# Kernel optimization log

Hardware: AMD Instinct MI355X
Metric: run time of the kernel (lower is better)

The kernel has to match this reference:

```python
import jax, jax.numpy as jnp
import numpy as np
import math

RCR = 5.2
RCA = 3.5
NUM_SPECIES = 4


def _triu_index(num_species):
    s1, s2 = np.triu_indices(num_species)
    ret = np.zeros((num_species, num_species), dtype=np.int32)
    ret[s1, s2] = np.arange(len(s1))
    ret[s2, s1] = np.arange(len(s1))
    return ret


def _cutoff_cosine(d, rc):
    return 0.5 * jnp.cos(d * (math.pi / rc)) + 0.5


def setup_inputs():
    key = jax.random.key(0)
    k1, k2 = jax.random.split(key)
    M, A = 32, 48
    BOX = 8.0  # ~0.43 atoms/A^3, realistic organic density
    coordinates = jax.random.uniform(k1, (M, A, 3), dtype=jnp.float32) * BOX
    species = jax.random.randint(k2, (M, A), 0, NUM_SPECIES)
    EtaR = jnp.array([16.0], dtype=jnp.float32)
    ShfR = jnp.asarray(0.9 + (RCR - 0.9) / 16.0 * np.arange(16), dtype=jnp.float32)
    EtaA = jnp.array([8.0], dtype=jnp.float32)
    Zeta = jnp.array([32.0], dtype=jnp.float32)
    ShfA = jnp.asarray(0.9 + (RCA - 0.9) / 4.0 * np.arange(4), dtype=jnp.float32)
    ShfZ = jnp.asarray((np.arange(8) + 0.5) * np.pi / 8.0, dtype=jnp.float32)
    return {"coordinates": coordinates, "EtaR": EtaR, "ShfR": ShfR,
            "EtaA": EtaA, "Zeta": Zeta, "ShfA": ShfA, "ShfZ": ShfZ,
            "species": species}


def _compute_aev(coordinates, EtaR, ShfR, EtaA, Zeta, ShfA, ShfZ, species):
    M, A, _ = coordinates.shape
    S = NUM_SPECIES
    npairs_sp = S * (S + 1) // 2  # 10 unordered species pairs
    rad_sub = EtaR.shape[0] * ShfR.shape[0]   # 16
    ang_sub = EtaA.shape[0] * Zeta.shape[0] * ShfA.shape[0] * ShfZ.shape[0]  # 32

    diff = coordinates[:, :, None, :] - coordinates[:, None, :, :]  # (M,A,A,3)
    D = jnp.linalg.norm(diff, axis=-1)                              # (M,A,A)
    mrow = jnp.arange(M)[:, None]

    # ---------- radial AEV (eq. 3) ----------
    p1, p2 = np.triu_indices(A, 1)                                  # static (P,)
    d = D[:, p1, p2]                                                # (M,P)
    mask_r = (d <= RCR).astype(d.dtype)
    du = d[:, :, None, None]                                        # (M,P,1,1)
    fc = _cutoff_cosine(du, RCR)
    rt = 0.25 * jnp.exp(-EtaR[:, None] * (du - ShfR[None, :]) ** 2) * fc
    rt = (rt * mask_r[:, :, None, None]).reshape(M, len(p1), rad_sub)
    sp = species
    idx1 = p1[None, :] * S + sp[:, p2]                              # (M,P)
    idx2 = p2[None, :] * S + sp[:, p1]
    radial = jnp.zeros((M, A * S, rad_sub), dtype=rt.dtype)
    radial = radial.at[mrow, idx1].add(rt).at[mrow, idx2].add(rt)
    radial = radial.reshape(M, A, S * rad_sub)

    # ---------- angular AEV (eq. 4) ----------
    # static triple list: central atom i with unordered neighbor pair (j,k), j,k != i
    jj, kk = np.triu_indices(A - 1, 1)
    tri = []
    for i in range(A):
        others = np.concatenate([np.arange(i), np.arange(i + 1, A)])
        tri.append(np.stack([np.full(jj.shape, i), others[jj], others[kk]], 1))
    tri = np.concatenate(tri)                                       # (T,3)
    ci, n1, n2 = tri[:, 0], tri[:, 1], tri[:, 2]

    v1 = coordinates[:, n1] - coordinates[:, ci]                    # (M,T,3)
    v2 = coordinates[:, n2] - coordinates[:, ci]
    d1 = D[:, ci, n1]
    d2 = D[:, ci, n2]
    mask_a = ((d1 <= RCA) & (d2 <= RCA)).astype(d1.dtype)           # (M,T)
    eps = 1e-8  # torch cosine_similarity eps
    cos = 0.95 * jnp.sum(v1 * v2, -1) / (jnp.maximum(d1, eps) * jnp.maximum(d2, eps))
    ang = jnp.arccos(cos)                                           # (M,T)

    # broadcast axes: (M, T, EtaA, Zeta, ShfA, ShfZ) as in torchani constants
    EtaA_b = EtaA.reshape(1, 1, -1, 1, 1, 1)
    Zeta_b = Zeta.reshape(1, 1, 1, -1, 1, 1)
    ShfA_b = ShfA.reshape(1, 1, 1, 1, -1, 1)
    ShfZ_b = ShfZ.reshape(1, 1, 1, 1, 1, -1)
    a6 = ang[:, :, None, None, None, None]
    dm = ((d1 + d2) / 2)[:, :, None, None, None, None]
    fcj = (_cutoff_cosine(d1, RCA) * _cutoff_cosine(d2, RCA))[:, :, None, None, None, None]
    f1 = ((1 + jnp.cos(a6 - ShfZ_b)) / 2) ** Zeta_b
    f2 = jnp.exp(-EtaA_b * (dm - ShfA_b) ** 2)
    at = (2 * f1 * f2 * fcj).reshape(M, tri.shape[0], ang_sub)
    at = at * mask_a[:, :, None]

    triu = jnp.asarray(_triu_index(S))
    pidx = triu[sp[:, n1], sp[:, n2]]                               # (M,T)
    flat = ci[None, :] * npairs_sp + pidx
    angular = jnp.zeros((M, A * npairs_sp, ang_sub), dtype=at.dtype)
    angular = angular.at[mrow, flat].add(at).reshape(M, A, npairs_sp * ang_sub)

    return jnp.concatenate([radial, angular], axis=-1)              # (M,A,384)


def reference(coordinates, EtaR, ShfR, EtaA, Zeta, ShfA, ShfZ, species):
    return _compute_aev(coordinates, EtaR, ShfR, EtaA, Zeta, ShfA, ShfZ, species)
```

## Files before the change

### kernel.cpp

```cpp
#include <hip/hip_runtime.h>
#include <hip/hip_bf16.h>


#define NA 48
#define RCR_F 5.2f
#define RCA_F 3.5f
#define PI_F 3.14159265358979f
#define LOG2E_F 1.44269504088896f
#define RADLEN 64
#define AEVLEN 384

struct Smem {
    float sx[NA], sy[NA], sz[NA];
    int   ssp[NA];
    float2 rab[NA];
    float ad[NA], avx[NA], avy[NA], avz[NA], afc[NA]; int asp[NA];
    int   nR, nAn;
    float4 pstage[256];
    int    bins[10], start[10];
    float rpart[4][64];
    float apart[4][320];
};

template <typename T> __device__ __forceinline__ float toF(const T* p, int i);
template <> __device__ __forceinline__ float toF<float>(const float* p, int i) { return p[i]; }
template <> __device__ __forceinline__ float toF<__hip_bfloat16>(const __hip_bfloat16* p, int i) { return __bfloat162float(p[i]); }

template <typename T> __device__ __forceinline__ void stF(T* p, size_t i, float v);
template <> __device__ __forceinline__ void stF<float>(float* p, size_t i, float v) { p[i] = v; }
template <> __device__ __forceinline__ void stF<__hip_bfloat16>(__hip_bfloat16* p, size_t i, float v) { p[i] = __float2bfloat16(v); }

__device__ __forceinline__ int triu_idx(int a, int b) {
    int lo = a < b ? a : b;
    int hi = a < b ? b : a;
    return lo * 4 - (lo * (lo - 1)) / 2 + (hi - lo);
}

template <typename T>
__device__ void aev_body(Smem& sm,
    const T* __restrict__ coords, const T* __restrict__ etaR_p,
    const T* __restrict__ shfR_p, const T* __restrict__ etaA_p,
    const T* __restrict__ zeta_p, const T* __restrict__ shfA_p,
    const T* __restrict__ shfZ_p, const int* __restrict__ species,
    T* __restrict__ out)
{
    const int tid  = threadIdx.x;
    const int lane = tid & 63;
    const int w    = tid >> 6;
    const int bid  = blockIdx.x;
    const int m  = bid / NA;
    const int ci = bid % NA;

    const float etaR = toF(etaR_p, 0);
    const float etaA = toF(etaA_p, 0);
    const float zeta = toF(zeta_p, 0);
    const float kR   = etaR * LOG2E_F;
    const float k2   = etaA * LOG2E_F;

    if (tid < NA) {
        int g = m * NA + tid;
        sm.sx[tid]  = toF(coords, 3 * g + 0);
        sm.sy[tid]  = toF(coords, 3 * g + 1);
        sm.sz[tid]  = toF(coords, 3 * g + 2);
        sm.ssp[tid] = species[g];
    }
    __syncthreads();

    if (w == 0) {
        const float cx = sm.sx[ci], cy = sm.sy[ci], cz = sm.sz[ci];
        float dx = 0.f, dy = 0.f, dz = 0.f, d = 1e30f;
        if (lane < NA && lane != ci) {
            dx = sm.sx[lane] - cx; dy = sm.sy[lane] - cy; dz = sm.sz[lane] - cz;
            d = sqrtf(dx * dx + dy * dy + dz * dz);
        }
        unsigned long long mR = __ballot(d <= RCR_F);
        unsigned long long mA = __ballot(d <= RCA_F);
        unsigned long long lanebit = 1ull << lane;
        unsigned long long below = lanebit - 1ull;
        if (mR & lanebit) {
            int s = __popcll(mR & below);
            float fcR = 0.5f * __cosf(d * (PI_F / RCR_F)) + 0.5f;
            float rb = fmaxf(__log2f(0.25f * fcR) - kR * d * d, -8.0e4f);
            unsigned rbu = (__float_as_uint(rb) & ~3u) | (unsigned)sm.ssp[lane];
            sm.rab[s] = make_float2(2.f * kR * d, __uint_as_float(rbu));
        }
        if (mA & lanebit) {
            int s = __popcll(mA & below);
            sm.ad[s]  = d;
            sm.avx[s] = dx; sm.avy[s] = dy; sm.avz[s] = dz;
            sm.afc[s] = 0.5f * __cosf(d * (PI_F / RCA_F)) + 0.5f;
            sm.asp[s] = sm.ssp[lane];
        }
        if (lane == 0) { sm.nR = (int)__popcll(mR); sm.nAn = (int)__popcll(mA); }
    }
    __syncthreads();

    const int nR  = sm.nR;
    const int nAn = sm.nAn;

    const float myShfR = toF(shfR_p, lane & 15);
    const int   mySp   = lane >> 4;
    const float myRc   = kR * myShfR * myShfR;
    const bool  z32    = (zeta == 32.f);

    float racc = 0.f;
    for (int i = w; i < nR; i += 4) {
        float2 rv = sm.rab[i];
        unsigned ru = __float_as_uint(rv.y);
        float arg = __builtin_fmaf(rv.x, myShfR, rv.y) - myRc;
        float t = __builtin_amdgcn_exp2f(arg);
        racc += ((int)(ru & 3u) == mySp) ? t : 0.f;
    }
    sm.rpart[w][lane] = racc;

    const int myA  = (lane >> 3) & 3;
    const int myZ  = lane & 7;
    const int p0   = lane >> 5;
    const float myShfA = toF(shfA_p, myA);
    const float myShfZ = toF(shfZ_p, myZ);
    const float myCz = __cosf(myShfZ);
    const float mySz = __sinf(myShfZ);
    const float myLc = k2 * myShfA * myShfA;

    float accs[5] = {0.f, 0.f, 0.f, 0.f, 0.f};
    const int np = nAn * (nAn - 1) / 2;

    for (int c0 = 0; c0 < np; c0 += 256) {
        const int nc = (np - c0 < 256) ? (np - c0) : 256;
        if (tid < 10) sm.bins[tid] = 0;
        __syncthreads();

        int myrow = -1, myrank = 0;
        float4 P4;
        if (tid < nc) {
            int p = c0 + tid;
            const int b = 2 * nAn - 1;
            float s = sqrtf((float)(b * b - 8 * p));
            int j = (int)(((float)b - s) * 0.5f);
            if ((j + 1) * (b - 1 - j) <= 2 * p) j++;
            if (j * (b - j) > 2 * p) j--;
            int k = p - ((j * (b - j)) >> 1) + j + 1;

            float d1 = sm.ad[j], d2 = sm.ad[k];
            float dot = sm.avx[j] * sm.avx[k] + sm.avy[j] * sm.avy[k] + sm.avz[j] * sm.avz[k];
            float cv = 0.95f * dot / (fmaxf(d1, 1e-8f) * fmaxf(d2, 1e-8f));
            float sv = sqrtf(fmaxf(1.f - cv * cv, 0.f));
            float dm = 0.5f * (d1 + d2);
            float fc2 = 2.f * sm.afc[j] * sm.afc[k];
            float pe = fmaxf(-k2 * dm * dm + __log2f(fc2), -8.0e4f);
            float pd = 2.f * k2 * dm;
            P4 = make_float4(cv, sv, pd, pe);
            myrow = triu_idx(sm.asp[j], sm.asp[k]);
            myrank = atomicAdd(&sm.bins[myrow], 1);
        }
        __syncthreads();
        if (tid == 0) {
            int s = 0;
            #pragma unroll
            for (int r = 0; r < 10; r++) { sm.start[r] = s; s += sm.bins[r]; }
        }
        __syncthreads();
        if (myrow >= 0) sm.pstage[sm.start[myrow] + myrank] = P4;
        __syncthreads();

        #pragma unroll
        for (int r = 0; r < 10; r++) {
            const int st = sm.start[r], cn = sm.bins[r];
            const int half = p0 ^ (r & 1);
            float tacc = 0.f;
            for (int o2 = 2 * w; o2 < cn; o2 += 8) {
                int ord = o2 + half;
                bool valid = ord < cn;
                float4 P = sm.pstage[st + (valid ? ord : o2)];
                float cd = __builtin_fmaf(P.x, myCz, P.y * mySz);
                float x = __builtin_fmaf(0.5f, cd, 0.5f);
                float f1;
                if (z32) { float x2 = x*x, x4 = x2*x2, x8 = x4*x4, x16 = x8*x8; f1 = x16*x16; }
                else     { f1 = __powf(x, zeta); }
                float term = f1 * __builtin_amdgcn_exp2f(
                                 __builtin_fmaf(P.z, myShfA, P.w - myLc));
                tacc += valid ? term : 0.f;
            }
            float other = __shfl_xor(tacc, 32);
            accs[r >> 1] += (half == 0) ? (tacc + other) : 0.f;
        }
        __syncthreads();
    }

    sm.apart[w][lane + 0]   = accs[0];
    sm.apart[w][lane + 64]  = accs[1];
    sm.apart[w][lane + 128] = accs[2];
    sm.apart[w][lane + 192] = accs[3];
    sm.apart[w][lane + 256] = accs[4];
    __syncthreads();

    const size_t ob = (size_t)bid * AEVLEN;
    if (tid < 64) {
        float r = sm.rpart[0][tid] + sm.rpart[1][tid] + sm.rpart[2][tid] + sm.rpart[3][tid];
        stF(out, ob + tid, r);
    }
    {
        float v = sm.apart[0][tid] + sm.apart[1][tid] + sm.apart[2][tid] + sm.apart[3][tid];
        stF(out, ob + RADLEN + tid, v);
    }
    if (tid < 64) {
        int s = 256 + tid;
        float v = sm.apart[0][s] + sm.apart[1][s] + sm.apart[2][s] + sm.apart[3][s];
        stF(out, ob + RADLEN + s, v);
    }
}

__global__ __launch_bounds__(256) void aev_kernel(
    const void* coords, const void* etaR, const void* shfR, const void* etaA,
    const void* zeta, const void* shfA, const void* shfZ,
    const int* __restrict__ species, void* out)
{
    __shared__ Smem sm;
    const float probe = __uint_as_float(((const unsigned int*)shfR)[0]);
    if (probe > 0.85f && probe < 0.95f) {
        aev_body<float>(sm, (const float*)coords, (const float*)etaR,
                        (const float*)shfR, (const float*)etaA, (const float*)zeta,
                        (const float*)shfA, (const float*)shfZ, species, (float*)out);
    } else {
        aev_body<__hip_bfloat16>(sm, (const __hip_bfloat16*)coords,
                        (const __hip_bfloat16*)etaR, (const __hip_bfloat16*)shfR,
                        (const __hip_bfloat16*)etaA, (const __hip_bfloat16*)zeta,
                        (const __hip_bfloat16*)shfA, (const __hip_bfloat16*)shfZ,
                        species, (__hip_bfloat16*)out);
    }
}

extern "C" void kernel_launch(void* const* d_in, const int* in_sizes, int n_in,
                              void* d_out, int out_size, void* d_ws, size_t ws_size,
                              hipStream_t stream) {
    aev_kernel<<<dim3(32 * NA), dim3(256), 0, stream>>>(
        d_in[0], d_in[1], d_in[2], d_in[3], d_in[4], d_in[5], d_in[6],
        (const int*)d_in[7], d_out);
}
```

Measured before the change: 75.90 us.

## Replace block-wide angular pair binning with per-wavefront ballot sorting

Each wavefront now takes its own 64-pair chunk of angular triples and sorts them by species pair using ballot/popcount prefix sums into a private staging buffer. This removes the shared-memory atomics and the four block-wide barriers per 256-pair chunk. Each wave then processes its own chunk fully rather than interleaving over a shared one. Load balance across waves may become uneven when the pair count is not a multiple of 256.

```diff
diff --git a/kernel.cpp b/kernel.cpp
--- a/kernel.cpp
+++ b/kernel.cpp
@@ -16,8 +16,7 @@
     float2 rab[NA];
     float ad[NA], avx[NA], avy[NA], avz[NA], afc[NA]; int asp[NA];
     int   nR, nAn;
-    float4 pstage[256];
-    int    bins[10], start[10];
+    float4 pstage[4][64];
     float rpart[4][64];
     float apart[4][320];
 };
@@ -121,19 +120,19 @@
     const float myCz = __cosf(myShfZ);
     const float mySz = __sinf(myShfZ);
     const float myLc = k2 * myShfA * myShfA;
+    const unsigned long long below = (1ull << lane) - 1ull;
 
     float accs[5] = {0.f, 0.f, 0.f, 0.f, 0.f};
     const int np = nAn * (nAn - 1) / 2;
-
-    for (int c0 = 0; c0 < np; c0 += 256) {
-        const int nc = (np - c0 < 256) ? (np - c0) : 256;
-        if (tid < 10) sm.bins[tid] = 0;
-        __syncthreads();
-
-        int myrow = -1, myrank = 0;
+    float4* const myStage = sm.pstage[w];
+
+    for (int c0 = 64 * w; c0 < np; c0 += 256) {
+        const int ncw = (np - c0 < 64) ? (np - c0) : 64;
+
+        int myrow = -1;
         float4 P4;
-        if (tid < nc) {
-            int p = c0 + tid;
+        if (lane < ncw) {
+            int p = c0 + lane;
             const int b = 2 * nAn - 1;
             float s = sqrtf((float)(b * b - 8 * p));
             int j = (int)(((float)b - s) * 0.5f);
@@ -151,27 +150,30 @@
             float pd = 2.f * k2 * dm;
             P4 = make_float4(cv, sv, pd, pe);
             myrow = triu_idx(sm.asp[j], sm.asp[k]);
-            myrank = atomicAdd(&sm.bins[myrow], 1);
-        }
-        __syncthreads();
-        if (tid == 0) {
-            int s = 0;
-            #pragma unroll
-            for (int r = 0; r < 10; r++) { sm.start[r] = s; s += sm.bins[r]; }
-        }
-        __syncthreads();
-        if (myrow >= 0) sm.pstage[sm.start[myrow] + myrank] = P4;
-        __syncthreads();
-
+        }
+
+        int cnR[10], stR[10];
+        int myslot = 0, cum = 0;
         #pragma unroll
         for (int r = 0; r < 10; r++) {
-            const int st = sm.start[r], cn = sm.bins[r];
+            unsigned long long mk = __ballot(myrow == r);
+            int c = (int)__popcll(mk);
+            stR[r] = cum;
+            cnR[r] = c;
+            if (myrow == r) myslot = cum + (int)__popcll(mk & below);
+            cum += c;
+        }
+        if (myrow >= 0) myStage[myslot] = P4;
+
+        #pragma unroll
+        for (int r = 0; r < 10; r++) {
+            const int st = stR[r], cn = cnR[r];
             const int half = p0 ^ (r & 1);
             float tacc = 0.f;
-            for (int o2 = 2 * w; o2 < cn; o2 += 8) {
+            for (int o2 = 0; o2 < cn; o2 += 2) {
                 int ord = o2 + half;
                 bool valid = ord < cn;
-                float4 P = sm.pstage[st + (valid ? ord : o2)];
+                float4 P = myStage[st + (valid ? ord : o2)];
                 float cd = __builtin_fmaf(P.x, myCz, P.y * mySz);
                 float x = __builtin_fmaf(0.5f, cd, 0.5f);
                 float f1;
@@ -184,7 +186,6 @@
             float other = __shfl_xor(tacc, 32);
             accs[r >> 1] += (half == 0) ? (tacc + other) : 0.f;
         }
-        __syncthreads();
     }
 
     sm.apart[w][lane + 0]   = accs[0];
```

Result: no change. 76.04 us (+0.2%).
